# Performance work log

Hardware: AMD Instinct MI355X
Metric: run time of the kernel (lower is better)

## Reference

```python
import jax, jax.numpy as jnp
import numpy as np

H = 16  # num_heads
D = 64  # head_dim


def setup_inputs() -> dict:
    key = jax.random.key(0)
    ks = jax.random.split(key, 9)
    B, S, E = 2, 2048, 1024
    scale = 1.0 / np.sqrt(E)
    return {
        "hidden_states": jax.random.normal(ks[0], (B, S, E), jnp.float32),
        "bias": jax.random.normal(ks[1], (1, H, S, S), jnp.float32) * 0.02,
        "Wq": jax.random.normal(ks[2], (E, E), jnp.float32) * scale,
        "bq": jax.random.normal(ks[3], (E,), jnp.float32) * 0.02,
        "Wk": jax.random.normal(ks[4], (E, E), jnp.float32) * scale,
        "bk": jax.random.normal(ks[5], (E,), jnp.float32) * 0.02,
        "Wv": jax.random.normal(ks[6], (E, E), jnp.float32) * scale,
        "bv": jax.random.normal(ks[7], (E,), jnp.float32) * 0.02,
        "Wo": jax.random.normal(ks[8], (E, E), jnp.float32) * scale,
    }


def _split_heads(x, B, S):
    # (B, S, E) -> (B, H, S, D)
    return x.reshape(B, S, H, D).transpose(0, 2, 1, 3)


def reference(hidden_states, bias, Wq, bq, Wk, bk, Wv, bv, Wo):
    B, S, E = hidden_states.shape
    # nn.Linear: y = x @ W^T + b
    q = _split_heads(hidden_states @ Wq.T + bq, B, S)
    k = _split_heads(hidden_states @ Wk.T + bk, B, S)
    v = _split_heads(hidden_states @ Wv.T + bv, B, S)
    scores = jnp.einsum("bhqd,bhkd->bhqk", q, k) / jnp.sqrt(jnp.asarray(D, q.dtype))
    scores = scores + bias  # bias [1,H,S,S] broadcasts over batch (matches .repeat)
    attn = jax.nn.softmax(scores, axis=-1)
    out = jnp.einsum("bhqk,bhkd->bhqd", attn, v)
    out = out.transpose(0, 2, 1, 3).reshape(B, S, E)
    return out @ Wo.T
```

## Files before the change

kernel.cpp:

```cpp
#include <hip/hip_runtime.h>
#include <hip/hip_bf16.h>


typedef __attribute__((ext_vector_type(8))) __bf16 bf16x8;
typedef __attribute__((ext_vector_type(4))) float f32x4;

__device__ __forceinline__ void gl2lds16(const void* g, void* l) {
    __builtin_amdgcn_global_load_lds(
        (const __attribute__((address_space(1))) void*)g,
        (__attribute__((address_space(3))) void*)l, 16, 0, 0);
}

__global__ __launch_bounds__(256) void prep(
    const float* __restrict__ hs, const float* __restrict__ Wq,
    const float* __restrict__ Wk, const float* __restrict__ Wv,
    const float* __restrict__ Wo,
    __bf16* __restrict__ hsb, __bf16* __restrict__ wqb, __bf16* __restrict__ wkb,
    __bf16* __restrict__ wvb, __bf16* __restrict__ wohb, __bf16* __restrict__ wolb)
{
    size_t i = (size_t)blockIdx.x * 256 + threadIdx.x;
    const float* s; __bf16 *d1, *d2 = nullptr; size_t off;
    if (i < 1048576)      { s = hs; d1 = hsb; off = i; }
    else if (i < 1310720) { s = Wq; d1 = wqb; off = i - 1048576; }
    else if (i < 1572864) { s = Wk; d1 = wkb; off = i - 1310720; }
    else if (i < 1835008) { s = Wv; d1 = wvb; off = i - 1572864; }
    else                  { s = Wo; d1 = wohb; d2 = wolb; off = i - 1835008; }
    float4 v = *(const float4*)(s + off * 4);
    union { __bf16 b[4]; uint2 u; } ph;
    ph.b[0] = (__bf16)v.x; ph.b[1] = (__bf16)v.y;
    ph.b[2] = (__bf16)v.z; ph.b[3] = (__bf16)v.w;
    *(uint2*)(d1 + off * 4) = ph.u;
    if (d2) {
        union { __bf16 b[4]; uint2 u; } pl;
        pl.b[0] = (__bf16)(v.x - (float)ph.b[0]);
        pl.b[1] = (__bf16)(v.y - (float)ph.b[1]);
        pl.b[2] = (__bf16)(v.z - (float)ph.b[2]);
        pl.b[3] = (__bf16)(v.w - (float)ph.b[3]);
        *(uint2*)(d2 + off * 4) = pl.u;
    }
}

__global__ __launch_bounds__(256, 3) void gemm_qkv(
    const __bf16* __restrict__ hsb, const __bf16* __restrict__ wqb,
    const __bf16* __restrict__ wkb, const __bf16* __restrict__ wvb,
    const float* __restrict__ bq, const float* __restrict__ bk, const float* __restrict__ bv,
    __bf16* __restrict__ qo, __bf16* __restrict__ ko, __bf16* __restrict__ vTo)
{
    __shared__ alignas(16) __bf16 As[128][32];
    __shared__ alignas(16) __bf16 Ws[128][32];
    const int tid = threadIdx.x;
    const int w = tid >> 6, lane = tid & 63, quad = lane >> 4, l = lane & 15;
    const int blk = blockIdx.x;
    const int proj = blk >> 8;
    const int loc = blk & 255;
    int bm, bn;
    const __bf16 *Ap, *Wp; const float* bp;
    if (proj == 0)      { Ap = hsb; Wp = wqb; bp = bq; bm = (loc >> 3) << 7; bn = (loc & 7) << 7; }
    else if (proj == 1) { Ap = hsb; Wp = wkb; bp = bk; bm = (loc >> 3) << 7; bn = (loc & 7) << 7; }
    else                { Ap = wvb; Wp = hsb; bp = bv; bm = (loc & 7) << 7; bn = (loc >> 3) << 7; }
    const int wm = (w >> 1) << 6, wn = (w & 1) << 6;
    const int seg_r = lane >> 2, seg_c = (lane & 3) << 3;

    f32x4 acc[4][4];
#pragma unroll
    for (int i = 0; i < 4; ++i)
#pragma unroll
        for (int j = 0; j < 4; ++j) acc[i][j] = f32x4{0.f, 0.f, 0.f, 0.f};

    for (int k0 = 0; k0 < 1024; k0 += 32) {
        __syncthreads();
#pragma unroll
        for (int j = 0; j < 2; ++j) {
            int seg = w * 2 + j;
            int row = seg * 16 + seg_r;
            gl2lds16(Ap + (size_t)(bm + row) * 1024 + k0 + seg_c,
                     (char*)As + seg * 1024 + lane * 16);
            gl2lds16(Wp + (size_t)(bn + row) * 1024 + k0 + seg_c,
                     (char*)Ws + seg * 1024 + lane * 16);
        }
        __syncthreads();
        bf16x8 af[4], bfr[4];
#pragma unroll
        for (int t = 0; t < 4; ++t) {
            af[t]  = *(const bf16x8*)&As[wm + t * 16 + l][quad * 8];
            bfr[t] = *(const bf16x8*)&Ws[wn + t * 16 + l][quad * 8];
        }
#pragma unroll
        for (int mt = 0; mt < 4; ++mt)
#pragma unroll
            for (int nt = 0; nt < 4; ++nt)
                acc[mt][nt] = __builtin_amdgcn_mfma_f32_16x16x32_bf16(
                    af[mt], bfr[nt], acc[mt][nt], 0, 0, 0);
    }

    if (proj < 2) {
        __bf16* dst = proj ? ko : qo;
        const float scale = proj ? 1.0f : 0.125f;
        float bcol[4];
#pragma unroll
        for (int nt = 0; nt < 4; ++nt) bcol[nt] = bp[bn + wn + nt * 16 + l];
#pragma unroll
        for (int mt = 0; mt < 4; ++mt)
#pragma unroll
            for (int r = 0; r < 4; ++r) {
                int m = bm + wm + mt * 16 + quad * 4 + r;
                int b_ = m >> 11, s = m & 2047;
#pragma unroll
                for (int nt = 0; nt < 4; ++nt) {
                    int n = bn + wn + nt * 16 + l;
                    int h = n >> 6, d = n & 63;
                    dst[(((size_t)(b_ * 16 + h) * 2048 + s) << 6) + d] =
                        (__bf16)((acc[mt][nt][r] + bcol[nt]) * scale);
                }
            }
    } else {
#pragma unroll
        for (int mt = 0; mt < 4; ++mt)
#pragma unroll
            for (int r = 0; r < 4; ++r) {
                int im = bm + wm + mt * 16 + quad * 4 + r;
                int h = im >> 6, d = im & 63;
                float bm_ = bp[im];
#pragma unroll
                for (int nt = 0; nt < 4; ++nt) {
                    int in = bn + wn + nt * 16 + l;
                    int b_ = in >> 11, s = in & 2047;
                    vTo[(((size_t)(b_ * 16 + h) * 64 + d) << 11) + s] =
                        (__bf16)(acc[mt][nt][r] + bm_);
                }
            }
    }
}

__global__ __launch_bounds__(256, 2) void flash_attn_mfma(
    const __bf16* __restrict__ q, const __bf16* __restrict__ k,
    const __bf16* __restrict__ vT, const float* __restrict__ bias,
    __bf16* __restrict__ attn_hi, __bf16* __restrict__ attn_lo)
{
    constexpr int S = 2048;
    __shared__ alignas(16) unsigned char smem[33792];
    __bf16 (*Ks)[64]  = (__bf16(*)[64])(smem);
    __bf16 (*VTs)[64] = (__bf16(*)[64])(smem + 8192);
    __bf16 (*Ps)[68]  = (__bf16(*)[68])(smem + 16384);
    __bf16 (*Qs)[64]  = (__bf16(*)[64])(smem + 16384);

    const int tid = threadIdx.x;
    const int b = blockIdx.x, h = blockIdx.y, qt = blockIdx.z;
    const int bh = b * 16 + h;
    const int q0 = qt * 128;
    const int w = tid >> 6, lane = tid & 63, quad = lane >> 4, l = lane & 15;

    const __bf16* Qp = q + ((size_t)bh * S + q0) * 64;
#pragma unroll
    for (int j = 0; j < 4; ++j) {
        int P = (w * 4 + j) * 64 + lane;
        int row = P >> 3, pblk = P & 7;
        int lblk = pblk ^ (row & 7);
        gl2lds16(Qp + row * 64 + lblk * 8, (char*)Qs + (size_t)P * 16);
    }
    __syncthreads();

    bf16x8 qf[2][2];
#pragma unroll
    for (int rt = 0; rt < 2; ++rt)
#pragma unroll
        for (int ks = 0; ks < 2; ++ks) {
            int row = w * 32 + rt * 16 + l;
            qf[rt][ks] = *(const bf16x8*)&Qs[row][((ks * 4 + quad) ^ (row & 7)) * 8];
        }

    float l_[2][4];
    f32x4 o_[2][4];
#pragma unroll
    for (int rt = 0; rt < 2; ++rt)
#pragma unroll
        for (int r = 0; r < 4; ++r) {
            l_[rt][r] = 0.0f;
            o_[rt][r] = f32x4{0.f, 0.f, 0.f, 0.f};
        }

    const __bf16* Kp0 = k + (size_t)bh * S * 64;
    const __bf16* Vp0 = vT + (size_t)bh * 64 * S;
    const float* Bp0 = bias + (size_t)h * S * S + (size_t)q0 * S;

    for (int kt = 0; kt < S / 64; ++kt) {
        f32x4 sc[2][4];
#pragma unroll
        for (int rt = 0; rt < 2; ++rt)
#pragma unroll
            for (int r = 0; r < 4; ++r) {
                const float* bp = Bp0 + (size_t)(w * 32 + rt * 16 + quad * 4 + r) * S
                                + kt * 64 + l;
#pragma unroll
                for (int ct = 0; ct < 4; ++ct) sc[rt][ct][r] = bp[ct * 16];
            }

        __syncthreads();
        const __bf16* Kt = Kp0 + kt * 64 * 64;
        const __bf16* Vt = Vp0 + kt * 64;
#pragma unroll
        for (int j = 0; j < 2; ++j) {
            int P = (w * 2 + j) * 64 + lane;
            int row = P >> 3, pblk = P & 7;
            int lblk = pblk ^ (row & 7);
            gl2lds16(Kt + row * 64 + lblk * 8,        (char*)Ks  + (size_t)P * 16);
            gl2lds16(Vt + (size_t)row * S + lblk * 8, (char*)VTs + (size_t)P * 16);
        }
        __syncthreads();

#pragma unroll
        for (int ct = 0; ct < 4; ++ct) {
            int krow = ct * 16 + l;
            bf16x8 b0 = *(const bf16x8*)&Ks[krow][((0 + quad) ^ (l & 7)) * 8];
            bf16x8 b1 = *(const bf16x8*)&Ks[krow][((4 + quad) ^ (l & 7)) * 8];
            sc[0][ct] = __builtin_amdgcn_mfma_f32_16x16x32_bf16(qf[0][0], b0, sc[0][ct], 0, 0, 0);
            sc[0][ct] = __builtin_amdgcn_mfma_f32_16x16x32_bf16(qf[0][1], b1, sc[0][ct], 0, 0, 0);
            sc[1][ct] = __builtin_amdgcn_mfma_f32_16x16x32_bf16(qf[1][0], b0, sc[1][ct], 0, 0, 0);
            sc[1][ct] = __builtin_amdgcn_mfma_f32_16x16x32_bf16(qf[1][1], b1, sc[1][ct], 0, 0, 0);
        }

#pragma unroll
        for (int rt = 0; rt < 2; ++rt)
#pragma unroll
            for (int r = 0; r < 4; ++r) {
                int row = w * 32 + rt * 16 + quad * 4 + r;
                float ps = 0.f;
#pragma unroll
                for (int ct = 0; ct < 4; ++ct) {
                    float p = __expf(sc[rt][ct][r] - 8.0f);
                    Ps[row][ct * 16 + l] = (__bf16)p;
                    ps += p;
                }
                l_[rt][r] += ps;
            }

#pragma unroll
        for (int ks = 0; ks < 2; ++ks) {
            bf16x8 pa0 = *(const bf16x8*)&Ps[w * 32 + l][ks * 32 + quad * 8];
            bf16x8 pa1 = *(const bf16x8*)&Ps[w * 32 + 16 + l][ks * 32 + quad * 8];
#pragma unroll
            for (int dt = 0; dt < 4; ++dt) {
                bf16x8 vb = *(const bf16x8*)&VTs[dt * 16 + l][((ks * 4 + quad) ^ (l & 7)) * 8];
                o_[0][dt] = __builtin_amdgcn_mfma_f32_16x16x32_bf16(pa0, vb, o_[0][dt], 0, 0, 0);
                o_[1][dt] = __builtin_amdgcn_mfma_f32_16x16x32_bf16(pa1, vb, o_[1][dt], 0, 0, 0);
            }
        }
    }

#pragma unroll
    for (int rt = 0; rt < 2; ++rt)
#pragma unroll
        for (int r = 0; r < 4; ++r) {
            float ps = l_[rt][r];
            ps += __shfl_xor(ps, 1);
            ps += __shfl_xor(ps, 2);
            ps += __shfl_xor(ps, 4);
            ps += __shfl_xor(ps, 8);
            float linv = 1.0f / ps;
            int row = q0 + w * 32 + rt * 16 + quad * 4 + r;
            size_t base = (size_t)(b * S + row) * 1024 + h * 64;
#pragma unroll
            for (int dt = 0; dt < 4; ++dt) {
                float x = o_[rt][dt][r] * linv;
                __bf16 hi = (__bf16)x;
                attn_hi[base + dt * 16 + l] = hi;
                attn_lo[base + dt * 16 + l] = (__bf16)(x - (float)hi);
            }
        }
}

__global__ __launch_bounds__(256, 3) void gemm_out(
    const __bf16* __restrict__ ah, const __bf16* __restrict__ al,
    const __bf16* __restrict__ wh, const __bf16* __restrict__ wl,
    float* __restrict__ C)
{
    __shared__ alignas(16) __bf16 Ah[64][32], Al[64][32];
    __shared__ alignas(16) __bf16 Wh[128][32], Wl[128][32];
    const int tid = threadIdx.x;
    const int w = tid >> 6, lane = tid & 63, quad = lane >> 4, l = lane & 15;
    const int bm = (int)(blockIdx.x >> 3) << 6;
    const int bn = (int)(blockIdx.x & 7) << 7;
    const int wm = (w >> 1) << 5, wn = (w & 1) << 6;
    const int seg_r = lane >> 2, seg_c = (lane & 3) << 3;

    f32x4 acc[2][4];
#pragma unroll
    for (int i = 0; i < 2; ++i)
#pragma unroll
        for (int j = 0; j < 4; ++j) acc[i][j] = f32x4{0.f, 0.f, 0.f, 0.f};

    for (int k0 = 0; k0 < 1024; k0 += 32) {
        __syncthreads();
        {
            int row = w * 16 + seg_r;
            gl2lds16(ah + (size_t)(bm + row) * 1024 + k0 + seg_c,
                     (char*)Ah + w * 1024 + lane * 16);
            gl2lds16(al + (size_t)(bm + row) * 1024 + k0 + seg_c,
                     (char*)Al + w * 1024 + lane * 16);
#pragma unroll
            for (int j = 0; j < 2; ++j) {
                int seg = w * 2 + j;
                int wrow = seg * 16 + seg_r;
                gl2lds16(wh + (size_t)(bn + wrow) * 1024 + k0 + seg_c,
                         (char*)Wh + seg * 1024 + lane * 16);
                gl2lds16(wl + (size_t)(bn + wrow) * 1024 + k0 + seg_c,
                         (char*)Wl + seg * 1024 + lane * 16);
            }
        }
        __syncthreads();
        bf16x8 ahf[2], alf[2], whf[4], wlf[4];
#pragma unroll
        for (int t = 0; t < 2; ++t) {
            ahf[t] = *(const bf16x8*)&Ah[wm + t * 16 + l][quad * 8];
            alf[t] = *(const bf16x8*)&Al[wm + t * 16 + l][quad * 8];
        }
#pragma unroll
        for (int t = 0; t < 4; ++t) {
            whf[t] = *(const bf16x8*)&Wh[wn + t * 16 + l][quad * 8];
            wlf[t] = *(const bf16x8*)&Wl[wn + t * 16 + l][quad * 8];
        }
#pragma unroll
        for (int mt = 0; mt < 2; ++mt)
#pragma unroll
            for (int nt = 0; nt < 4; ++nt) {
                acc[mt][nt] = __builtin_amdgcn_mfma_f32_16x16x32_bf16(ahf[mt], whf[nt], acc[mt][nt], 0, 0, 0);
                acc[mt][nt] = __builtin_amdgcn_mfma_f32_16x16x32_bf16(ahf[mt], wlf[nt], acc[mt][nt], 0, 0, 0);
                acc[mt][nt] = __builtin_amdgcn_mfma_f32_16x16x32_bf16(alf[mt], whf[nt], acc[mt][nt], 0, 0, 0);
            }
    }

#pragma unroll
    for (int mt = 0; mt < 2; ++mt)
#pragma unroll
        for (int r = 0; r < 4; ++r) {
            int m = bm + wm + mt * 16 + quad * 4 + r;
#pragma unroll
            for (int nt = 0; nt < 4; ++nt)
                C[(size_t)m * 1024 + bn + wn + nt * 16 + l] = acc[mt][nt][r];
        }
}

extern "C" void kernel_launch(void* const* d_in, const int* in_sizes, int n_in,
                              void* d_out, int out_size, void* d_ws, size_t ws_size,
                              hipStream_t stream) {
    const float* hs   = (const float*)d_in[0];
    const float* bias = (const float*)d_in[1];
    const float* Wq   = (const float*)d_in[2];
    const float* bq   = (const float*)d_in[3];
    const float* Wk   = (const float*)d_in[4];
    const float* bk   = (const float*)d_in[5];
    const float* Wv   = (const float*)d_in[6];
    const float* bv   = (const float*)d_in[7];
    const float* Wo   = (const float*)d_in[8];
    float* out = (float*)d_out;
    char* ws = (char*)d_ws;

    __bf16* attn_hi = (__bf16*)(ws);
    __bf16* attn_lo = (__bf16*)(ws + ((size_t) 8 << 20));
    __bf16* qb      = (__bf16*)(ws + ((size_t)16 << 20));
    __bf16* kb      = (__bf16*)(ws + ((size_t)24 << 20));
    __bf16* vTb     = (__bf16*)(ws + ((size_t)32 << 20));
    __bf16* hsb     = (__bf16*)(ws + ((size_t)40 << 20));
    __bf16* wqb     = (__bf16*)(ws + ((size_t)48 << 20));
    __bf16* wkb     = (__bf16*)(ws + ((size_t)50 << 20));
    __bf16* wvb     = (__bf16*)(ws + ((size_t)52 << 20));
    __bf16* wohb    = (__bf16*)(ws + ((size_t)54 << 20));
    __bf16* wolb    = (__bf16*)(ws + ((size_t)56 << 20));

    prep<<<8192, 256, 0, stream>>>(hs, Wq, Wk, Wv, Wo, hsb, wqb, wkb, wvb, wohb, wolb);

    gemm_qkv<<<768, 256, 0, stream>>>(hsb, wqb, wkb, wvb, bq, bk, bv, qb, kb, vTb);

    dim3 fg(2, 16, 16);
    flash_attn_mfma<<<fg, 256, 0, stream>>>(qb, kb, vTb, bias, attn_hi, attn_lo);

    gemm_out<<<512, 256, 0, stream>>>(attn_hi, attn_lo, wohb, wolb, out);
}
```

Measured before the change: 507.6 us.

## Double-buffer K/V tiles and prefetch bias in flash attention loop

The attention kernel now keeps two LDS buffers for the K and V^T tiles. It issues the next tile's global-to-LDS loads and the next bias register loads before computing the current tile, so memory latency overlaps with MFMA work. The two syncthreads per iteration become a single barrier at the end of the loop. It also raises wave priority around the MFMA blocks with s_setprio. LDS use rises to about 49KB per block and register pressure rises from the prefetched bias values, which could hurt occupancy.

```diff
diff --git a/kernel.cpp b/kernel.cpp
--- a/kernel.cpp
+++ b/kernel.cpp
@@ -138,11 +138,9 @@
     __bf16* __restrict__ attn_hi, __bf16* __restrict__ attn_lo)
 {
     constexpr int S = 2048;
-    __shared__ alignas(16) unsigned char smem[33792];
-    __bf16 (*Ks)[64]  = (__bf16(*)[64])(smem);
-    __bf16 (*VTs)[64] = (__bf16(*)[64])(smem + 8192);
-    __bf16 (*Ps)[68]  = (__bf16(*)[68])(smem + 16384);
-    __bf16 (*Qs)[64]  = (__bf16(*)[64])(smem + 16384);
+    constexpr int NT = S / 64;
+    __shared__ alignas(16) unsigned char smem[50176];
+    __bf16 (*Ps)[68] = (__bf16(*)[68])(smem + 32768);
 
     const int tid = threadIdx.x;
     const int b = blockIdx.x, h = blockIdx.y, qt = blockIdx.z;
@@ -150,64 +148,100 @@
     const int q0 = qt * 128;
     const int w = tid >> 6, lane = tid & 63, quad = lane >> 4, l = lane & 15;
 
-    const __bf16* Qp = q + ((size_t)bh * S + q0) * 64;
-#pragma unroll
-    for (int j = 0; j < 4; ++j) {
-        int P = (w * 4 + j) * 64 + lane;
-        int row = P >> 3, pblk = P & 7;
-        int lblk = pblk ^ (row & 7);
-        gl2lds16(Qp + row * 64 + lblk * 8, (char*)Qs + (size_t)P * 16);
-    }
-    __syncthreads();
-
-    bf16x8 qf[2][2];
-#pragma unroll
-    for (int rt = 0; rt < 2; ++rt)
-#pragma unroll
-        for (int ks = 0; ks < 2; ++ks) {
-            int row = w * 32 + rt * 16 + l;
-            qf[rt][ks] = *(const bf16x8*)&Qs[row][((ks * 4 + quad) ^ (row & 7)) * 8];
-        }
-
-    float l_[2][4];
-    f32x4 o_[2][4];
-#pragma unroll
-    for (int rt = 0; rt < 2; ++rt)
-#pragma unroll
-        for (int r = 0; r < 4; ++r) {
-            l_[rt][r] = 0.0f;
-            o_[rt][r] = f32x4{0.f, 0.f, 0.f, 0.f};
-        }
-
     const __bf16* Kp0 = k + (size_t)bh * S * 64;
     const __bf16* Vp0 = vT + (size_t)bh * 64 * S;
-    const float* Bp0 = bias + (size_t)h * S * S + (size_t)q0 * S;
-
-    for (int kt = 0; kt < S / 64; ++kt) {
-        f32x4 sc[2][4];
-#pragma unroll
-        for (int rt = 0; rt < 2; ++rt)
-#pragma unroll
-            for (int r = 0; r < 4; ++r) {
-                const float* bp = Bp0 + (size_t)(w * 32 + rt * 16 + quad * 4 + r) * S
-                                + kt * 64 + l;
-#pragma unroll
-                for (int ct = 0; ct < 4; ++ct) sc[rt][ct][r] = bp[ct * 16];
-            }
-
-        __syncthreads();
-        const __bf16* Kt = Kp0 + kt * 64 * 64;
-        const __bf16* Vt = Vp0 + kt * 64;
+    const float*  Bp0 = bias + (size_t)h * S * S + (size_t)q0 * S;
+
+    {
+        const __bf16* Qp = q + ((size_t)bh * S + q0) * 64;
+#pragma unroll
+        for (int j = 0; j < 4; ++j) {
+            int P = (w * 4 + j) * 64 + lane;
+            int row = P >> 3, pblk = P & 7;
+            int lblk = pblk ^ (row & 7);
+            gl2lds16(Qp + row * 64 + lblk * 8, (char*)smem + 32768 + (size_t)P * 16);
+        }
 #pragma unroll
         for (int j = 0; j < 2; ++j) {
             int P = (w * 2 + j) * 64 + lane;
             int row = P >> 3, pblk = P & 7;
             int lblk = pblk ^ (row & 7);
-            gl2lds16(Kt + row * 64 + lblk * 8,        (char*)Ks  + (size_t)P * 16);
-            gl2lds16(Vt + (size_t)row * S + lblk * 8, (char*)VTs + (size_t)P * 16);
-        }
-        __syncthreads();
-
+            gl2lds16(Kp0 + row * 64 + lblk * 8,        (char*)smem + (size_t)P * 16);
+            gl2lds16(Vp0 + (size_t)row * S + lblk * 8, (char*)smem + 16384 + (size_t)P * 16);
+        }
+    }
+
+    f32x4 pf[2][4];
+#pragma unroll
+    for (int rt = 0; rt < 2; ++rt)
+#pragma unroll
+        for (int r = 0; r < 4; ++r) {
+            const float* bp = Bp0 + (size_t)(w * 32 + rt * 16 + quad * 4 + r) * S + l;
+#pragma unroll
+            for (int ct = 0; ct < 4; ++ct) pf[rt][ct][r] = bp[ct * 16];
+        }
+
+    __syncthreads();
+
+    bf16x8 qf[2][2];
+    {
+        const __bf16 (*Qs)[64] = (const __bf16(*)[64])(smem + 32768);
+#pragma unroll
+        for (int rt = 0; rt < 2; ++rt)
+#pragma unroll
+            for (int ks = 0; ks < 2; ++ks) {
+                int row = w * 32 + rt * 16 + l;
+                qf[rt][ks] = *(const bf16x8*)&Qs[row][((ks * 4 + quad) ^ (row & 7)) * 8];
+            }
+    }
+    __syncthreads();
+
+    float l_[2][4];
+    f32x4 o_[2][4];
+#pragma unroll
+    for (int rt = 0; rt < 2; ++rt)
+#pragma unroll
+        for (int r = 0; r < 4; ++r) {
+            l_[rt][r] = 0.0f;
+            o_[rt][r] = f32x4{0.f, 0.f, 0.f, 0.f};
+        }
+
+    for (int kt = 0; kt < NT; ++kt) {
+        const int cur = kt & 1;
+        const __bf16 (*Ks)[64]  = (const __bf16(*)[64])(smem + cur * 8192);
+        const __bf16 (*VTs)[64] = (const __bf16(*)[64])(smem + 16384 + cur * 8192);
+
+        f32x4 sc[2][4];
+#pragma unroll
+        for (int rt = 0; rt < 2; ++rt)
+#pragma unroll
+            for (int ct = 0; ct < 4; ++ct) sc[rt][ct] = pf[rt][ct];
+
+        if (kt + 1 < NT) {
+            const __bf16* Kt = Kp0 + (kt + 1) * 64 * 64;
+            const __bf16* Vt = Vp0 + (kt + 1) * 64;
+            char* Kd = (char*)smem + (cur ^ 1) * 8192;
+            char* Vd = (char*)smem + 16384 + (cur ^ 1) * 8192;
+#pragma unroll
+            for (int j = 0; j < 2; ++j) {
+                int P = (w * 2 + j) * 64 + lane;
+                int row = P >> 3, pblk = P & 7;
+                int lblk = pblk ^ (row & 7);
+                gl2lds16(Kt + row * 64 + lblk * 8,        Kd + (size_t)P * 16);
+                gl2lds16(Vt + (size_t)row * S + lblk * 8, Vd + (size_t)P * 16);
+            }
+            const float* Bn = Bp0 + (kt + 1) * 64;
+#pragma unroll
+            for (int rt = 0; rt < 2; ++rt)
+#pragma unroll
+                for (int r = 0; r < 4; ++r) {
+                    const float* bp = Bn + (size_t)(w * 32 + rt * 16 + quad * 4 + r) * S + l;
+#pragma unroll
+                    for (int ct = 0; ct < 4; ++ct) pf[rt][ct][r] = bp[ct * 16];
+                }
+        }
+
+        __builtin_amdgcn_s_setprio(1);
 #pragma unroll
         for (int ct = 0; ct < 4; ++ct) {
             int krow = ct * 16 + l;
@@ -218,6 +252,7 @@
             sc[1][ct] = __builtin_amdgcn_mfma_f32_16x16x32_bf16(qf[1][0], b0, sc[1][ct], 0, 0, 0);
             sc[1][ct] = __builtin_amdgcn_mfma_f32_16x16x32_bf16(qf[1][1], b1, sc[1][ct], 0, 0, 0);
         }
+        __builtin_amdgcn_s_setprio(0);
 
 #pragma unroll
         for (int rt = 0; rt < 2; ++rt)
@@ -234,6 +269,7 @@
                 l_[rt][r] += ps;
             }
 
+        __builtin_amdgcn_s_setprio(1);
 #pragma unroll
         for (int ks = 0; ks < 2; ++ks) {
             bf16x8 pa0 = *(const bf16x8*)&Ps[w * 32 + l][ks * 32 + quad * 8];
@@ -245,6 +281,9 @@
                 o_[1][dt] = __builtin_amdgcn_mfma_f32_16x16x32_bf16(pa1, vb, o_[1][dt], 0, 0, 0);
             }
         }
+        __builtin_amdgcn_s_setprio(0);
+
+        __syncthreads();
     }
 
 #pragma unroll
```

New measurement: 508.8 us. Within noise of the previous version (+0.2%).
